# Optimization experiments

Hardware: AMD Instinct MI355X
Metric: run time of the kernel (lower is better)

## Reference

```python
import jax, jax.numpy as jnp
import numpy as np

B, L = 128, 128            # batch, num_features (sequence length)
D_MODEL = 256
D_INNER = 512              # expand=2
D_STATE = 16
D_CONV = 4
DT_RANK = 16               # ceil(d_model/16)
N_LAYERS = 2
LN_EPS = 1e-5


def setup_inputs() -> dict:
    key = jax.random.key(0)
    ks = jax.random.split(key, 12)
    rn = lambda k, shp, s=0.02: (jax.random.normal(k, shp, jnp.float32) * s)
    A_init = jnp.tile(jnp.arange(1, D_STATE + 1, dtype=jnp.float32), (N_LAYERS, D_INNER, 1))
    return {
        "x_num": jax.random.normal(ks[0], (B, L), jnp.float32),
        "scalar_w": rn(ks[1], (D_MODEL, 1), 0.5),
        "scalar_b": jnp.zeros((D_MODEL,), jnp.float32),
        "in_proj_w": rn(ks[2], (N_LAYERS, 2 * D_INNER, D_MODEL)),
        "conv_w": rn(ks[3], (N_LAYERS, D_INNER, D_CONV), 0.2),
        "conv_b": jnp.zeros((N_LAYERS, D_INNER), jnp.float32),
        "x_proj_w": rn(ks[4], (N_LAYERS, DT_RANK + 2 * D_STATE, D_INNER)),
        "dt_proj_w": rn(ks[5], (N_LAYERS, D_INNER, DT_RANK), 0.1),
        "dt_proj_b": jnp.full((N_LAYERS, D_INNER), float(np.log(np.expm1(0.01))), jnp.float32),
        "A_log": jnp.log(A_init),
        "D_skip": jnp.ones((N_LAYERS, D_INNER), jnp.float32),
        "out_proj_w": rn(ks[6], (N_LAYERS, D_MODEL, D_INNER)),
        "ln_g": jnp.ones((D_MODEL,), jnp.float32),
        "ln_b": jnp.zeros((D_MODEL,), jnp.float32),
        "h1_w": rn(ks[7], (D_MODEL, D_MODEL)),
        "h1_b": jnp.zeros((D_MODEL,), jnp.float32),
        "h2_w": rn(ks[8], (1, D_MODEL)),
        "h2_b": jnp.zeros((1,), jnp.float32),
    }


def _selective_scan(u, delta, A, Bm, C, D_skip):
    # u, delta: [B,L,Di]; A: [Di,N]; Bm, C: [B,L,N]
    deltaA = jnp.exp(jnp.einsum('bld,dn->bldn', delta, A))          # [B,L,Di,N]
    deltaBu = jnp.einsum('bld,bln,bld->bldn', delta, Bm, u)          # [B,L,Di,N]
    h0 = jnp.zeros((u.shape[0], u.shape[2], A.shape[1]), u.dtype)

    def step(h, inp):
        dA_t, dBu_t, c_t = inp
        h = dA_t * h + dBu_t                                         # [B,Di,N]
        y = jnp.einsum('bdn,bn->bd', h, c_t)
        return h, y

    _, ys = jax.lax.scan(
        step, h0,
        (deltaA.transpose(1, 0, 2, 3), deltaBu.transpose(1, 0, 2, 3), C.transpose(1, 0, 2)))
    return ys.transpose(1, 0, 2) + u * D_skip                        # [B,L,Di]


def _mamba_block(x, Wi, cw, cb, Wx, Wdt, bdt, A_log, Dsk, Wo):
    xz = jnp.einsum('bld,ed->ble', x, Wi)                            # [B,L,2*Di]
    xh, z = jnp.split(xz, 2, axis=-1)
    # causal depthwise conv1d, kernel D_CONV
    xt = xh.transpose(0, 2, 1)                                       # [B,Di,L]
    conv = jax.lax.conv_general_dilated(
        xt, cw[:, None, :], window_strides=(1,), padding=[(D_CONV - 1, 0)],
        feature_group_count=D_INNER)
    xh = jax.nn.silu((conv + cb[:, None]).transpose(0, 2, 1))        # [B,L,Di]
    x_dbl = jnp.einsum('bld,ed->ble', xh, Wx)                        # [B,L,DT_RANK+2N]
    dt, Bm, C = jnp.split(x_dbl, [DT_RANK, DT_RANK + D_STATE], axis=-1)
    delta = jax.nn.softplus(jnp.einsum('blr,dr->bld', dt, Wdt) + bdt)
    A = -jnp.exp(A_log)
    y = _selective_scan(xh, delta, A, Bm, C, Dsk)
    y = y * jax.nn.silu(z)
    return jnp.einsum('bld,od->blo', y, Wo)                          # [B,L,D_MODEL]


def reference(x_num, scalar_w, scalar_b, in_proj_w, conv_w, conv_b, x_proj_w,
              dt_proj_w, dt_proj_b, A_log, D_skip, out_proj_w, ln_g, ln_b,
              h1_w, h1_b, h2_w, h2_b):
    # scalar_proj: Linear(1, d_model) applied to each feature value
    x = x_num[:, :, None] * scalar_w[:, 0] + scalar_b                # [B,L,D_MODEL]
    for i in range(N_LAYERS):
        x = _mamba_block(x, in_proj_w[i], conv_w[i], conv_b[i], x_proj_w[i],
                         dt_proj_w[i], dt_proj_b[i], A_log[i], D_skip[i], out_proj_w[i])
    mu = x.mean(-1, keepdims=True)
    var = ((x - mu) ** 2).mean(-1, keepdims=True)
    x = (x - mu) * jax.lax.rsqrt(var + LN_EPS) * ln_g + ln_b
    pooled = x.mean(axis=1)                                          # [B,D_MODEL]
    h = jax.nn.gelu(pooled @ h1_w.T + h1_b, approximate=False)
    return (h @ h2_w.T + h2_b)[:, 0]                                 # [B]
```

## Files before the change

### kernel.cpp

```cpp
#include <hip/hip_runtime.h>
#include <math.h>

#define BB 128
#define LL 128
#define DM 256
#define DI 512
#define NS 16
#define MR (BB*LL)
#define SC 8
#define ST 16
#define EPAD 34

typedef unsigned short u16;
typedef __attribute__((ext_vector_type(8))) short bf16x8;
typedef __attribute__((ext_vector_type(8))) short us8;
typedef __attribute__((ext_vector_type(4))) short u16x4;
typedef __attribute__((ext_vector_type(4))) float f32x4;
typedef __attribute__((ext_vector_type(2))) float f32x2;

__device__ __forceinline__ u16 f2bf(float v) {
    unsigned u = __float_as_uint(v);
    return (u16)((u + 0x7fffu + ((u >> 16) & 1u)) >> 16);
}
__device__ __forceinline__ u16 ftoh(float v) {
    _Float16 h = (_Float16)v;
    return __builtin_bit_cast(unsigned short, h);
}
__device__ __forceinline__ float htof(u16 x) {
    return (float)__builtin_bit_cast(_Float16, x);
}

__device__ __forceinline__ void g2l16(const u16* g, u16* l) {
    __builtin_amdgcn_global_load_lds(
        (const __attribute__((address_space(1))) void*)g,
        (__attribute__((address_space(3))) void*)l,
        16, 0, 0);
}

__device__ __forceinline__ void unpack8(const f32x4& a, const f32x4& b,
                                        const f32x4& c, const f32x4& d, f32x2* o) {
    o[0]=(f32x2){a[0],a[1]}; o[1]=(f32x2){a[2],a[3]};
    o[2]=(f32x2){b[0],b[1]}; o[3]=(f32x2){b[2],b[3]};
    o[4]=(f32x2){c[0],c[1]}; o[5]=(f32x2){c[2],c[3]};
    o[6]=(f32x2){d[0],d[1]}; o[7]=(f32x2){d[2],d[3]};
}

__device__ __forceinline__ void pow_tree2(float r, f32x2* p2) {
    float q = r*r, s = q*q, t = s*s;
    p2[0] = (f32x2){r, q};
    f32x2 qq = (f32x2){q, q}, ss = (f32x2){s, s}, tt = (f32x2){t, t};
    p2[1] = p2[0]*qq;
    p2[2] = p2[0]*ss;
    p2[3] = p2[1]*ss;
    p2[4] = p2[0]*tt;
    p2[5] = p2[1]*tt;
    p2[6] = p2[2]*tt;
    p2[7] = p2[3]*tt;
}

__device__ __forceinline__ void store8h(const float* v, u16* dh) {
    bf16x8 hv;
    #pragma unroll
    for (int j = 0; j < 8; j++) hv[j] = (short)f2bf(v[j]);
    *(bf16x8*)dh = hv;
}

__device__ __forceinline__ void unswz(int id, int NB, int& nb, int& mb) {
    int low = id & 7, rest = id >> 3;
    nb = rest % NB;
    mb = ((rest / NB) << 3) | low;
}

__device__ __forceinline__ void ldfA(const u16* gA, int t, int quad, int wm, int r16,
                                     bf16x8* fa) {
    const u16* p = gA + (size_t)((t*4 + quad)*128)*8;
    #pragma unroll
    for (int mt = 0; mt < 4; mt++)
        fa[mt] = *(const bf16x8*)(p + (size_t)(wm*64 + mt*16 + r16)*8);
}
__device__ __forceinline__ void ldfB(const u16* gB, int t, int quad, int wn, int boff,
                                     int r16, bf16x8* fb) {
    const u16* p = gB + (size_t)((t*4 + quad)*128 + boff)*8;
    #pragma unroll
    for (int nt = 0; nt < 2; nt++)
        fb[nt] = *(const bf16x8*)(p + (size_t)(wn*32 + nt*16 + r16)*8);
}

#define NCI  32768
#define NCXT 8192
#define NCDT 2048
#define NCO  16384
#define NCZ  32768
#define NPREP_PACK (NCI + 2*NCXT + 2*NCDT + 2*NCO + NCZ)
#define PREP_BLOCKS (NPREP_PACK/256 + 512)
#define OFF_WI1  0
#define OFF_WXT0 262144
#define OFF_WXT1 327680
#define OFF_WDT0 393216
#define OFF_WDT1 409600
#define OFF_WO1  425984
#define OFF_WOT0 557056
__global__ __launch_bounds__(256) void k_prep(
    const float* __restrict__ sw, const float* __restrict__ sbias,
    const float* __restrict__ Wi_all, const float* __restrict__ Wx_all,
    const float* __restrict__ Wdt_all, const float* __restrict__ Wo_all,
    u16* __restrict__ wbase, u16* __restrict__ t16, float* __restrict__ wvbv)
{
    int gc = blockIdx.x * 256 + threadIdx.x;
    float v[8];
    u16* dh;
    if (gc < NCI) {
        int c = gc, m = c & 127, t = c >> 7, kc = t & 31, rb = t >> 5;
        const float* Wi = Wi_all + (size_t)1024*256;
        const float* p = Wi + (size_t)(rb*128 + m)*256 + kc*8;
        float4 a = *(const float4*)p, b = *(const float4*)(p+4);
        v[0]=a.x; v[1]=a.y; v[2]=a.z; v[3]=a.w; v[4]=b.x; v[5]=b.y; v[6]=b.z; v[7]=b.w;
        dh = wbase + OFF_WI1 + (size_t)c*8;
    } else if (gc < NCI + 2*NCXT) {
        int c = gc - NCI; int layer = (c >= NCXT); c -= layer*NCXT;
        int m = c & 127, kc = c >> 7;
        const float* Wx = Wx_all + (size_t)layer*48*512;
        #pragma unroll
        for (int j = 0; j < 8; j++) v[j] = (m < 48) ? Wx[(size_t)m*512 + kc*8 + j] : 0.f;
        dh = wbase + (layer ? OFF_WXT1 : OFF_WXT0) + (size_t)c*8;
    } else if (gc < NCI + 2*NCXT + 2*NCDT) {
        int c = gc - NCI - 2*NCXT; int layer = (c >= NCDT); c -= layer*NCDT;
        int m = c & 127, t = c >> 7, kc = t & 3, rb = t >> 2;
        int d = rb*128 + m;
        const float* Wdt = Wdt_all + (size_t)layer*512*16;
        #pragma unroll
        for (int j = 0; j < 8; j++) {
            int r = kc*8 + j;
            v[j] = (r < 16) ? Wdt[d*16 + r] : 0.f;
        }
        dh = wbase + (layer ? OFF_WDT1 : OFF_WDT0) + (size_t)c*8;
    } else if (gc < NCI + 2*NCXT + 2*NCDT + NCO) {
        int c = gc - NCI - 2*NCXT - 2*NCDT;
        int m = c & 127, t = c >> 7, kc = t & 63, rb = t >> 6;
        const float* Wo = Wo_all + (size_t)256*512;
        const float* p = Wo + (size_t)(rb*128 + m)*512 + kc*8;
        float4 a = *(const float4*)p, b = *(const float4*)(p+4);
        v[0]=a.x; v[1]=a.y; v[2]=a.z; v[3]=a.w; v[4]=b.x; v[5]=b.y; v[6]=b.z; v[7]=b.w;
        dh = wbase + OFF_WO1 + (size_t)c*8;
    } else if (gc < NCI + 2*NCXT + 2*NCDT + 2*NCO) {
        int c = gc - NCI - 2*NCXT - 2*NCDT - NCO;
        int m = c & 127, t = c >> 7, kc = t & 31, rb = t >> 5;
        int d = rb*128 + m;
        const float* Wo = Wo_all;
        #pragma unroll
        for (int j = 0; j < 8; j++) v[j] = Wo[(size_t)(kc*8 + j)*512 + d];
        dh = wbase + OFF_WOT0 + (size_t)c*8;
    } else if (gc < NPREP_PACK) {
        int c = gc - (NCI + 2*NCXT + 2*NCDT + 2*NCO);
        int mb = c >> 8, rem = c & 255;
        #pragma unroll
        for (int j = 0; j < 8; j++) v[j] = 0.f;
        dh = t16 + ((size_t)(mb*4 + 2)*128 + rem)*8;
    } else {
        int wb   = blockIdx.x - NPREP_PACK/256;
        int o    = wb*4 + (threadIdx.x >> 6);
        int lane = threadIdx.x & 63;
        int isB  = o >> 10, e = o & 1023;
        const float* vec = isB ? sbias : sw;
        const float* row = Wi_all + (size_t)e*256;
        float4 w4 = *(const float4*)&row[lane*4];
        float4 v4 = *(const float4*)&vec[lane*4];
        float a = w4.x*v4.x + w4.y*v4.y + w4.z*v4.z + w4.w*v4.w;
        #pragma unroll
        for (int off = 32; off > 0; off >>= 1) a += __shfl_down(a, off, 64);
        if (lane == 0) wvbv[isB*1024 + e] = a;
        return;
    }
    store8h(v, dh);
}

__global__ __launch_bounds__(256) void k_front0(
    const float* __restrict__ xn, const float* __restrict__ wvbv,
    const float* __restrict__ cw, const float* __restrict__ cb,
    u16* __restrict__ Yh, u16* __restrict__ u2, u16* __restrict__ z2)
{
    const int id = blockIdx.x;
    const int low = id & 7, rest = id >> 3;
    const int seg = rest >> 4;
    const int b   = ((rest & 15) << 3) | low;
    const int tid = threadIdx.x;
    const int l = tid & 127, sub = tid >> 7;
    const float* xb = xn + (size_t)b * LL;
    const float x0  = xb[l];
    const float xm1 = (l >= 1) ? xb[l-1] : 0.f;
    const float xm2 = (l >= 2) ? xb[l-2] : 0.f;
    const float xm3 = (l >= 3) ? xb[l-3] : 0.f;
    const float* wv = wvbv;
    const float* bv = wvbv + 1024;
    if (seg < 4) {
        const int kcb = (seg*128 + sub*64) >> 3;
        #pragma unroll 1
        for (int kk = 0; kk < 8; kk++) {
            const int kc = kcb + kk;
            float uv[8];
            #pragma unroll
            for (int q = 0; q < 8; q++) {
                int d = kc*8 + q;
                float4 c4 = *(const float4*)&cw[d*4];
                float conv = c4.x*xm3 + c4.y*xm2 + c4.z*xm1 + c4.w*x0;
                float cs = c4.w;
                if (l >= 1) cs += c4.z;
                if (l >= 2) cs += c4.y;
                if (l >= 3) cs += c4.x;
                float s = wv[d]*conv + bv[d]*cs + cb[d];
                float sig = 1.f/(1.f + __expf(-s));
                uv[q] = s*sig;
                u2[((size_t)b*512 + d)*128 + l] = ftoh(uv[q]);
            }
            store8h(uv, &Yh[(((size_t)b*64 + kc)*128 + l)*8]);
        }
    } else {
        const int d0 = (seg - 4)*128 + sub*64;
        #pragma unroll 1
        for (int dd = 0; dd < 64; dd++) {
            int d = d0 + dd;
            float s = x0*wv[512 + d] + bv[512 + d];
            z2[((size_t)b*512 + d)*128 + l] = ftoh(s);
        }
    }
}

template<int CM>
__global__ __launch_bounds__(256) void k_gemm_mfma(
    const u16* __restrict__ Ah, const u16* __restrict__ Bh,
    void* __restrict__ Cv, void* __restrict__ C2v,
    const float* __restrict__ bdt,
    int K, int Nvalid, int nsplit, int ldc, int ldc2, int NB)
{
    const int tid = threadIdx.x, lane = tid & 63, w = tid >> 6;
    const int wm = w >> 1, wn = w & 1;
    const int r16 = lane & 15, quad = lane >> 4;
    int nb, mb;
    unswz(blockIdx.x, NB, nb, mb);
    const int K8 = K >> 3;
    const int NT = K >> 5;

    f32x4 acc[4][2];
    #pragma unroll
    for (int mt = 0; mt < 4; mt++)
        #pragma unroll
        for (int nt = 0; nt < 2; nt++) acc[mt][nt] = (f32x4){0.f,0.f,0.f,0.f};

    const u16* gAh = Ah + (size_t)mb * K8 * 128 * 8;
    const int rbB = nb >> 1, boff = (nb & 1) * 64;
    const u16* gBh = Bh + (size_t)rbB * K8 * 128 * 8;

    bf16x8 fa0[4], fb0[2], fa1[4], fb1[2];
    ldfA(gAh, 0, quad, wm, r16, fa0);
    ldfB(gBh, 0, quad, wn, boff, r16, fb0);
    for (int t = 0; t < NT; t += 2) {
        if (t + 1 < NT) {
            ldfA(gAh, t+1, quad, wm, r16, fa1);
            ldfB(gBh, t+1, quad, wn, boff, r16, fb1);
        }
        #pragma unroll
        for (int mt = 0; mt < 4; mt++)
            #pragma unroll
            for (int nt = 0; nt < 2; nt++)
                acc[mt][nt] = __builtin_amdgcn_mfma_f32_16x16x32_bf16(fa0[mt], fb0[nt], acc[mt][nt], 0, 0, 0);
        if (t + 2 < NT) {
            ldfA(gAh, t+2, quad, wm, r16, fa0);
            ldfB(gBh, t+2, quad, wn, boff, r16, fb0);
        }
        if (t + 1 < NT) {
            #pragma unroll
            for (int mt = 0; mt < 4; mt++)
                #pragma unroll
                for (int nt = 0; nt < 2; nt++)
                    acc[mt][nt] = __builtin_amdgcn_mfma_f32_16x16x32_bf16(fa1[mt], fb1[nt], acc[mt][nt], 0, 0, 0);
        }
    }

    const int col0 = nb*64 + wn*32;
    #pragma unroll
    for (int mt = 0; mt < 4; mt++) {
        int lrow = wm*64 + mt*16 + quad*4;
        int rowb = mb*128 + lrow;
        #pragma unroll
        for (int nt = 0; nt < 2; nt++) {
            int col = col0 + nt*16 + r16;
            if (col < Nvalid) {
                if (CM != 2 && col >= nsplit) {
                    float* Cd = (float*)C2v; int cc = col - nsplit;
                    #pragma unroll
                    for (int r = 0; r < 4; r++)
                        Cd[(size_t)(rowb + r)*ldc2 + cc] = acc[mt][nt][r];
                } else if (CM == 1) {
                    u16* Cd = (u16*)Cv;
                    float bv = bdt[col];
                    u16x4 pd;
                    #pragma unroll
                    for (int r = 0; r < 4; r++) {
                        float v    = acc[mt][nt][r] + bv;
                        float expv = __expf(v);
                        float dlt  = (v > 20.f) ? v : __logf(1.f + expv);
                        pd[r] = (short)ftoh(dlt);
                    }
                    *(u16x4*)&Cd[((size_t)mb*512 + col)*128 + lrow] = pd;
                } else if (CM == 2) {
                    u16* Dh = (u16*)Cv;
                    size_t cb = ((size_t)mb*(size_t)ldc + (col>>3))*1024 + (col&7);
                    #pragma unroll
                    for (int r = 0; r < 4; r++)
                        Dh[cb + (size_t)(lrow + r)*8] = f2bf(acc[mt][nt][r]);
                } else if (CM == 3) {
                    u16* Dh = (u16*)Cv;
                    size_t cb = (size_t)mb*4096 + (size_t)(col>>3)*1024 + (col&7);
                    #pragma unroll
                    for (int r = 0; r < 4; r++)
                        Dh[cb + (size_t)(lrow + r)*8] = f2bf(acc[mt][nt][r]);
                } else {
                    float* Cd = (float*)Cv;
                    #pragma unroll
                    for (int r = 0; r < 4; r++)
                        Cd[(size_t)(rowb + r)*ldc + col] = acc[mt][nt][r];
                }
            }
        }
    }
}

__global__ __launch_bounds__(256) void k_gemm_in(
    const u16* __restrict__ Ah, const u16* __restrict__ Bh,
    const float* __restrict__ cw, const float* __restrict__ cb,
    u16* __restrict__ Yh, u16* __restrict__ u2, u16* __restrict__ z2, int K8c)
{
    __shared__ __align__(16) char smem[24576];
    u16* sAh = (u16*)smem;
    u16* sBh = (u16*)(smem + 16384);

    const int tid = threadIdx.x, lane = tid & 63, w = tid >> 6;
    const int wm = w >> 1, wn = w & 1;
    const int r16 = lane & 15, quad = lane >> 4;
    int nb, mb;
    unswz(blockIdx.x, 16, nb, mb);
    const int NT = K8c >> 2;

    f32x4 acc[4][2];
    #pragma unroll
    for (int mt = 0; mt < 4; mt++)
        #pragma unroll
        for (int nt = 0; nt < 2; nt++) acc[mt][nt] = (f32x4){0.f,0.f,0.f,0.f};

    const u16* gAh = Ah + (size_t)mb * K8c * 128 * 8;
    const int rbB = nb >> 1, boff = (nb & 1) * 64;
    const u16* gBh = Bh + (size_t)rbB * K8c * 128 * 8;

    {
        #pragma unroll
        for (int t = 0; t < 2; t++) {
            int s = w + t * 4;
            g2l16(gAh + (size_t)(s*64 + lane)*8, &sAh[(s*64 + lane)*8]);
        }
        g2l16(gBh + ((size_t)w*128 + boff + lane)*8, &sBh[(w*64 + lane)*8]);
    }

    int cur = 0;
    for (int t = 0; t < NT; t++) {
        __syncthreads();
        if (t + 1 < NT) {
            const int kc0 = (t + 1) * 4;
            const u16* ga = gAh + (size_t)kc0 * 128 * 8;
            u16* dA = sAh + (cur ^ 1) * 4096;
            u16* dB = sBh + (cur ^ 1) * 2048;
            #pragma unroll
            for (int tt = 0; tt < 2; tt++) {
                int s = w + tt * 4;
                g2l16(ga + (size_t)(s*64 + lane)*8, &dA[(s*64 + lane)*8]);
            }
            g2l16(gBh + ((size_t)(kc0 + w)*128 + boff + lane)*8, &dB[(w*64 + lane)*8]);
        }

        const u16* rA = sAh + cur * 4096;
        const u16* rB = sBh + cur * 2048;
        bf16x8 fa_h[4], fb_h[2];
        #pragma unroll
        for (int mt = 0; mt < 4; mt++) {
            int ch = quad*128 + wm*64 + mt*16 + r16;
            fa_h[mt] = *(const bf16x8*)&rA[ch*8];
        }
        #pragma unroll
        for (int nt = 0; nt < 2; nt++) {
            int ch = quad*64 + wn*32 + nt*16 + r16;
            fb_h[nt] = *(const bf16x8*)&rB[ch*8];
        }
        #pragma unroll
        for (int mt = 0; mt < 4; mt++)
            #pragma unroll
            for (int nt = 0; nt < 2; nt++)
                acc[mt][nt] = __builtin_amdgcn_mfma_f32_16x16x32_bf16(fa_h[mt], fb_h[nt], acc[mt][nt], 0, 0, 0);
        cur ^= 1;
    }

    if (nb < 8) {
        float* eps = (float*)smem;
        float* scw = (float*)(smem + 17408);
        float* scb = (float*)(smem + 18432);
        __syncthreads();
        if (tid < 256) scw[tid] = cw[nb*256 + tid];
        if (tid < 64)  scb[tid] = cb[nb*64 + tid];

        #pragma unroll
        for (int rr = 0; rr < 2; rr++) {
            if (wn == rr) {
                #pragma unroll
                for (int mt = 0; mt < 4; mt++) {
                    int rbase = wm*64 + mt*16 + quad*4;
                    #pragma unroll
                    for (int ntl = 0; ntl < 2; ntl++) {
                        int ct = ntl*16 + r16;
                        #pragma unroll
                        for (int r = 0; r < 4; r++)
                            eps[(rbase + r)*EPAD + ct] = acc[mt][ntl][r];
                    }
                }
            }
            __syncthreads();
            #pragma unroll
            for (int t = 0; t < 2; t++) {
                int l  = (tid & 31) + ((tid >> 5) & 3) * 32;
                int oo = (tid >> 7) + t*2;
                int dl_ = rr*32 + oo*8;
                float xr[4][8];
                #pragma unroll
                for (int r2 = 0; r2 < 4; r2++) {
                    int row = l - 3 + r2;
                    if (row >= 0) {
                        const float2* p = (const float2*)&eps[row*EPAD + oo*8];
                        float2 a = p[0], b2 = p[1], c2 = p[2], d2 = p[3];
                        xr[r2][0]=a.x; xr[r2][1]=a.y; xr[r2][2]=b2.x; xr[r2][3]=b2.y;
                        xr[r2][4]=c2.x; xr[r2][5]=c2.y; xr[r2][6]=d2.x; xr[r2][7]=d2.y;
                    } else {
                        #pragma unroll
                        for (int j = 0; j < 8; j++) xr[r2][j] = 0.f;
                    }
                }
                float uv[8];
                #pragma unroll
                for (int j = 0; j < 8; j++) {
                    int dj = dl_ + j;
                    float4 w4 = *(const float4*)&scw[dj*4];
                    float s = scb[dj] + w4.x*xr[0][j] + w4.y*xr[1][j]
                                      + w4.z*xr[2][j] + w4.w*xr[3][j];
                    float sig = 1.f/(1.f + __expf(-s));
                    uv[j] = s*sig;
                }
                int d = nb*64 + dl_;
                size_t base = ((size_t)(mb*64 + (d>>3))*128 + l)*8;
                store8h(uv, &Yh[base]);
                #pragma unroll
                for (int j = 0; j < 8; j++)
                    u2[((size_t)mb*512 + d + j)*128 + l] = ftoh(uv[j]);
            }
            __syncthreads();
        }
    } else {
        const int col0 = (nb-8)*64 + wn*32;
        #pragma unroll
        for (int mt = 0; mt < 4; mt++) {
            int lb = wm*64 + mt*16 + quad*4;
            #pragma unroll
            for (int nt = 0; nt < 2; nt++) {
                int d = col0 + nt*16 + r16;
                u16x4 pk;
                #pragma unroll
                for (int r = 0; r < 4; r++) pk[r] = (short)ftoh(acc[mt][nt][r]);
                *(u16x4*)&z2[((size_t)mb*512 + d)*128 + lb] = pk;
            }
        }
    }
}

__global__ __launch_bounds__(512, 8) void k_scan_fused(
    const u16* __restrict__ dls, const float* __restrict__ bc,
    const u16* __restrict__ uu, const u16* __restrict__ zz,
    const float* __restrict__ Dsk, u16* __restrict__ Yh)
{
    __shared__ float sR[SC][64];
    __shared__ float sH[SC][64*17];
    const int tid  = threadIdx.x;
    const int lane = tid & 63;
    const int c    = __builtin_amdgcn_readfirstlane(tid >> 6);
    const int id   = blockIdx.x;
    const int low  = id & 7, rest = id >> 3;
    const int dgrp = rest >> 4;
    const int b    = ((rest & 15) << 3) | low;
    const int d    = dgrp*64 + lane;
    const int l0   = c*ST;

    const float dsk = Dsk[d];
    const size_t tb = ((size_t)b*512 + d)*128 + l0;
    const u16* pd = dls + tb;
    const u16* up = uu + tb;
    const u16* zp = zz + tb;
    const size_t ybase = ((size_t)(b*64 + (d>>3))*128 + l0)*8 + (d&7);
    const float* bp = bc + ((size_t)b*LL + l0)*32;

    f32x2 h2[8];
    #pragma unroll
    for (int n = 0; n < 8; n++) h2[n] = (f32x2){0.f, 0.f};
    float R = 1.f;

    #pragma unroll 1
    for (int t8 = 0; t8 < ST/8; t8++) {
        us8 vd = *(const us8*)(pd + t8*8);
        us8 vu = *(const us8*)(up + t8*8);
        #pragma unroll
        for (int j = 0; j < 8; j++) {
            int t = t8*8 + j;
            const float* bpt = bp + t*32;
            f32x4 qa = *(const f32x4*)(bpt);
            f32x4 qb = *(const f32x4*)(bpt + 4);
            f32x4 qc = *(const f32x4*)(bpt + 8);
            f32x4 qd = *(const f32x4*)(bpt + 12);
            f32x2 bvv[8];
            unpack8(qa, qb, qc, qd, bvv);
            float dlt = htof((u16)vd[j]);
            float r1  = __expf(-dlt);
            float du  = dlt * htof((u16)vu[j]);
            R *= r1;
            f32x2 p2[8];
            pow_tree2(r1, p2);
            f32x2 du2 = (f32x2){du, du};
            #pragma unroll
            for (int n = 0; n < 8; n++) h2[n] = p2[n]*h2[n] + bvv[n]*du2;
        }
    }

    sR[c][lane] = R;
    #pragma unroll
    for (int n = 0; n < 8; n++) {
        sH[c][lane*17 + 2*n]     = h2[n][0];
        sH[c][lane*17 + 2*n + 1] = h2[n][1];
    }
    __syncthreads();
    f32x2 hin2[8];
    #pragma unroll
    for (int n = 0; n < 8; n++) hin2[n] = (f32x2){0.f, 0.f};
    for (int cc = 0; cc < c; cc++) {
        float Rv = sR[cc][lane];
        f32x2 P2[8];
        pow_tree2(Rv, P2);
        #pragma unroll
        for (int n = 0; n < 8; n++) {
            f32x2 Sv = (f32x2){sH[cc][lane*17 + 2*n], sH[cc][lane*17 + 2*n + 1]};
            hin2[n] = P2[n]*hin2[n] + Sv;
        }
    }

    #pragma unroll
    for (int n = 0; n < 8; n++) h2[n] = hin2[n];

    u16* ph = Yh + ybase;

    #pragma unroll 1
    for (int t8 = 0; t8 < ST/8; t8++) {
        us8 vd = *(const us8*)(pd + t8*8);
        us8 vu = *(const us8*)(up + t8*8);
        us8 vz = *(const us8*)(zp + t8*8);
        #pragma unroll
        for (int j = 0; j < 8; j++) {
            int t = t8*8 + j;
            const float* bpt = bp + t*32;
            f32x4 qa = *(const f32x4*)(bpt);
            f32x4 qb = *(const f32x4*)(bpt + 4);
            f32x4 qc = *(const f32x4*)(bpt + 8);
            f32x4 qd = *(const f32x4*)(bpt + 12);
            f32x4 qe = *(const f32x4*)(bpt + 16);
            f32x4 qf = *(const f32x4*)(bpt + 20);
            f32x4 qg = *(const f32x4*)(bpt + 24);
            f32x4 qh = *(const f32x4*)(bpt + 28);
            f32x2 bvv[8], cvv[8];
            unpack8(qa, qb, qc, qd, bvv);
            unpack8(qe, qf, qg, qh, cvv);
            float dlt = htof((u16)vd[j]);
            float r1  = __expf(-dlt);
            float u   = htof((u16)vu[j]);
            float zv  = htof((u16)vz[j]);
            float du  = dlt * u;
            f32x2 p2[8];
            pow_tree2(r1, p2);
            f32x2 du2 = (f32x2){du, du};
            f32x2 yv2 = (f32x2){0.f, 0.f};
            #pragma unroll
            for (int n = 0; n < 8; n++) {
                h2[n] = p2[n]*h2[n] + bvv[n]*du2;
                yv2  += h2[n]*cvv[n];
            }
            float yv = yv2[0] + yv2[1] + u * dsk;
            float sig = 1.f/(1.f + __expf(-zv));
            float yg = yv * (zv * sig);
            ph[(size_t)t*8] = f2bf(yg);
        }
    }
}

__global__ __launch_bounds__(256) void k_ln_head(const float* __restrict__ x,
    const float* __restrict__ g, const float* __restrict__ bt,
    const float* __restrict__ h1w, const float* __restrict__ h1b,
    const float* __restrict__ h2w, const float* __restrict__ h2b,
    float* __restrict__ out)
{
    __shared__ float4 part[4][64];
    __shared__ float sp[DM];
    __shared__ float sred[DM];
    int b = blockIdx.x, tid = threadIdx.x, wave = tid >> 6, lane = tid & 63;
    const float4* xp = (const float4*)(x + (size_t)b*LL*DM);
    float4 acc = make_float4(0.f, 0.f, 0.f, 0.f);
    for (int i = 0; i < 32; i++) {
        int l = wave*32 + i;
        float4 v = xp[l*64 + lane];
        float s  = v.x + v.y + v.z + v.w;
        float s2 = v.x*v.x + v.y*v.y + v.z*v.z + v.w*v.w;
        #pragma unroll
        for (int off = 32; off > 0; off >>= 1) {
            s  += __shfl_down(s,  off, 64);
            s2 += __shfl_down(s2, off, 64);
        }
        s  = __shfl(s,  0, 64);
        s2 = __shfl(s2, 0, 64);
        float mu  = s  * (1.f/DM);
        float var = s2 * (1.f/DM) - mu*mu;
        float rs  = rsqrtf(var + 1e-5f);
        acc.x += (v.x - mu)*rs;
        acc.y += (v.y - mu)*rs;
        acc.z += (v.z - mu)*rs;
        acc.w += (v.w - mu)*rs;
    }
    part[wave][lane] = acc;
    __syncthreads();
    if (wave == 0) {
        float4 a0 = part[0][lane], a1 = part[1][lane], a2 = part[2][lane], a3 = part[3][lane];
        float4 gv = ((const float4*)g)[lane];
        float4 bv = ((const float4*)bt)[lane];
        float4 o;
        o.x = (a0.x+a1.x+a2.x+a3.x)*(1.f/LL)*gv.x + bv.x;
        o.y = (a0.y+a1.y+a2.y+a3.y)*(1.f/LL)*gv.y + bv.y;
        o.z = (a0.z+a1.z+a2.z+a3.z)*(1.f/LL)*gv.z + bv.z;
        o.w = (a0.w+a1.w+a2.w+a3.w)*(1.f/LL)*gv.w + bv.w;
        *(float4*)&sp[lane*4] = o;
    }
    __syncthreads();
    int j = tid;
    float a = h1b[j];
    const float* wr = &h1w[(size_t)j*DM];
    for (int m = 0; m < DM; m += 4) {
        float4 w4 = *(const float4*)&wr[m];
        a += sp[m]*w4.x + sp[m+1]*w4.y + sp[m+2]*w4.z + sp[m+3]*w4.w;
    }
    float hg = 0.5f*a*(1.f + erff(a*0.70710678118654752440f));
    sred[j] = hg * h2w[j];
    __syncthreads();
    for (int s = 128; s > 0; s >>= 1) {
        if (j < s) sred[j] += sred[j+s];
        __syncthreads();
    }
    if (j == 0) out[b] = sred[0] + h2b[0];
}

extern "C" void kernel_launch(void* const* d_in, const int* in_sizes, int n_in,
                              void* d_out, int out_size, void* d_ws, size_t ws_size,
                              hipStream_t stream)
{
    const float* x_num    = (const float*)d_in[0];
    const float* scalar_w = (const float*)d_in[1];
    const float* scalar_b = (const float*)d_in[2];
    const float* in_proj  = (const float*)d_in[3];
    const float* conv_w   = (const float*)d_in[4];
    const float* conv_b   = (const float*)d_in[5];
    const float* x_proj   = (const float*)d_in[6];
    const float* dt_w     = (const float*)d_in[7];
    const float* dt_b     = (const float*)d_in[8];
    const float* D_skip   = (const float*)d_in[10];
    const float* out_proj = (const float*)d_in[11];
    const float* ln_g     = (const float*)d_in[12];
    const float* ln_b     = (const float*)d_in[13];
    const float* h1_w     = (const float*)d_in[14];
    const float* h1_b     = (const float*)d_in[15];
    const float* h2_w     = (const float*)d_in[16];
    const float* h2_b     = (const float*)d_in[17];
    float* out = (float*)d_out;

    float* ws      = (float*)d_ws;
    float* x_buf   = ws;
    float* xh_raw  = x_buf  + (size_t)MR*DM;
    float* z_buf   = xh_raw + (size_t)MR*DI;
    float* xh      = z_buf  + (size_t)MR*DI;
    float* xdbl    = xh     + (size_t)MR*DI;
    float* wsplit  = xdbl   + (size_t)MR*48;

    u16* u2   = (u16*)(xh + (size_t)MR*256);
    u16* AhX  = (u16*)xh_raw;
    u16* z2   = (u16*)z_buf;
    u16* Yh1  = (u16*)z_buf + (size_t)MR*512;
    u16* dl2  = (u16*)x_buf;
    float* bc = xdbl;
    u16* t16  = (u16*)(xdbl + (size_t)MR*32);

    u16* wbase   = (u16*)wsplit;
    float* extra = wsplit + 344064;
    u16* Wcomb   = (u16*)extra;
    float* wvbv  = extra + 262144;

    const int BIG = 1 << 30;

    k_prep<<<PREP_BLOCKS, 256, 0, stream>>>(
        scalar_w, scalar_b, in_proj, x_proj, dt_w, out_proj, wbase, t16, wvbv);

    k_gemm_mfma<2><<<64, 256, 0, stream>>>(
        wbase + OFF_WI1, wbase + OFF_WOT0, (void*)Wcomb, (void*)0, (const float*)0,
        256, 512, BIG, 64 , 0, 8);

    k_front0<<<BB*8, 256, 0, stream>>>(
        x_num, wvbv, conv_w, conv_b, AhX, u2, z2);

    k_gemm_mfma<3><<<128, 256, 0, stream>>>(
        AhX, wbase + OFF_WXT0, (void*)t16, (void*)bc, (const float*)0,
        512, 48, 16, 0, 32, 1);
    k_gemm_mfma<1><<<8*BB, 256, 0, stream>>>(
        t16, wbase + OFF_WDT0, (void*)dl2, (void*)0, dt_b,
        32, 512, BIG, 512, 32, 8);

    k_scan_fused<<<BB*8, 512, 0, stream>>>(dl2, bc, u2, z2, D_skip, AhX);

    k_gemm_in<<<16*BB, 256, 0, stream>>>(
        AhX, Wcomb, conv_w + (size_t)DI*4, conv_b + DI,
        Yh1, u2, z2, 64);

    k_gemm_mfma<3><<<128, 256, 0, stream>>>(
        Yh1, wbase + OFF_WXT1, (void*)t16, (void*)bc, (const float*)0,
        512, 48, 16, 0, 32, 1);
    k_gemm_mfma<1><<<8*BB, 256, 0, stream>>>(
        t16, wbase + OFF_WDT1, (void*)dl2, (void*)0, dt_b + DI,
        32, 512, BIG, 512, 32, 8);

    k_scan_fused<<<BB*8, 512, 0, stream>>>(dl2, bc, u2, z2, D_skip + DI, AhX);

    k_gemm_mfma<0><<<4*BB, 256, 0, stream>>>(
        AhX, wbase + OFF_WO1, (void*)x_buf, (void*)x_buf, (const float*)0,
        512, 256, BIG, 256, 256, 4);

    k_ln_head<<<BB, 256, 0, stream>>>(x_buf, ln_g, ln_b, h1_w, h1_b, h2_w, h2_b, out);
}
```

Baseline: 293.7 us.

## Fuse dt projection and softplus into selective scan kernel

Drops the separate MFMA GEMM that computed delta (dt_proj plus softplus) into a bf16 buffer. The x_proj GEMM now writes the dt-rank features as fp32, and each scan thread computes its 16 delta values with a rank-16 dot product against its dt_proj row. It also derives exp(-delta) as 1/(1+e^v), which saves one exp. This removes a kernel launch per layer and a delta round-trip through memory, at the cost of recomputing delta in both scan passes and more per-thread loads and registers.

```diff
diff --git a/kernel.cpp b/kernel.cpp
--- a/kernel.cpp
+++ b/kernel.cpp
@@ -88,23 +88,19 @@
 
 #define NCI  32768
 #define NCXT 8192
-#define NCDT 2048
 #define NCO  16384
-#define NCZ  32768
-#define NPREP_PACK (NCI + 2*NCXT + 2*NCDT + 2*NCO + NCZ)
+#define NPREP_PACK (NCI + 2*NCXT + 2*NCO)
 #define PREP_BLOCKS (NPREP_PACK/256 + 512)
 #define OFF_WI1  0
 #define OFF_WXT0 262144
 #define OFF_WXT1 327680
-#define OFF_WDT0 393216
-#define OFF_WDT1 409600
-#define OFF_WO1  425984
-#define OFF_WOT0 557056
+#define OFF_WO1  393216
+#define OFF_WOT0 524288
 __global__ __launch_bounds__(256) void k_prep(
     const float* __restrict__ sw, const float* __restrict__ sbias,
     const float* __restrict__ Wi_all, const float* __restrict__ Wx_all,
-    const float* __restrict__ Wdt_all, const float* __restrict__ Wo_all,
-    u16* __restrict__ wbase, u16* __restrict__ t16, float* __restrict__ wvbv)
+    const float* __restrict__ Wo_all,
+    u16* __restrict__ wbase, float* __restrict__ wvbv)
 {
     int gc = blockIdx.x * 256 + threadIdx.x;
     float v[8];
@@ -123,39 +119,22 @@
         #pragma unroll
         for (int j = 0; j < 8; j++) v[j] = (m < 48) ? Wx[(size_t)m*512 + kc*8 + j] : 0.f;
         dh = wbase + (layer ? OFF_WXT1 : OFF_WXT0) + (size_t)c*8;
-    } else if (gc < NCI + 2*NCXT + 2*NCDT) {
-        int c = gc - NCI - 2*NCXT; int layer = (c >= NCDT); c -= layer*NCDT;
-        int m = c & 127, t = c >> 7, kc = t & 3, rb = t >> 2;
-        int d = rb*128 + m;
-        const float* Wdt = Wdt_all + (size_t)layer*512*16;
-        #pragma unroll
-        for (int j = 0; j < 8; j++) {
-            int r = kc*8 + j;
-            v[j] = (r < 16) ? Wdt[d*16 + r] : 0.f;
-        }
-        dh = wbase + (layer ? OFF_WDT1 : OFF_WDT0) + (size_t)c*8;
-    } else if (gc < NCI + 2*NCXT + 2*NCDT + NCO) {
-        int c = gc - NCI - 2*NCXT - 2*NCDT;
+    } else if (gc < NCI + 2*NCXT + NCO) {
+        int c = gc - NCI - 2*NCXT;
         int m = c & 127, t = c >> 7, kc = t & 63, rb = t >> 6;
         const float* Wo = Wo_all + (size_t)256*512;
         const float* p = Wo + (size_t)(rb*128 + m)*512 + kc*8;
         float4 a = *(const float4*)p, b = *(const float4*)(p+4);
         v[0]=a.x; v[1]=a.y; v[2]=a.z; v[3]=a.w; v[4]=b.x; v[5]=b.y; v[6]=b.z; v[7]=b.w;
         dh = wbase + OFF_WO1 + (size_t)c*8;
-    } else if (gc < NCI + 2*NCXT + 2*NCDT + 2*NCO) {
-        int c = gc - NCI - 2*NCXT - 2*NCDT - NCO;
+    } else if (gc < NPREP_PACK) {
+        int c = gc - NCI - 2*NCXT - NCO;
         int m = c & 127, t = c >> 7, kc = t & 31, rb = t >> 5;
         int d = rb*128 + m;
         const float* Wo = Wo_all;
         #pragma unroll
         for (int j = 0; j < 8; j++) v[j] = Wo[(size_t)(kc*8 + j)*512 + d];
         dh = wbase + OFF_WOT0 + (size_t)c*8;
-    } else if (gc < NPREP_PACK) {
-        int c = gc - (NCI + 2*NCXT + 2*NCDT + 2*NCO);
-        int mb = c >> 8, rem = c & 255;
-        #pragma unroll
-        for (int j = 0; j < 8; j++) v[j] = 0.f;
-        dh = t16 + ((size_t)(mb*4 + 2)*128 + rem)*8;
     } else {
         int wb   = blockIdx.x - NPREP_PACK/256;
         int o    = wb*4 + (threadIdx.x >> 6);
@@ -229,7 +208,6 @@
 __global__ __launch_bounds__(256) void k_gemm_mfma(
     const u16* __restrict__ Ah, const u16* __restrict__ Bh,
     void* __restrict__ Cv, void* __restrict__ C2v,
-    const float* __restrict__ bdt,
     int K, int Nvalid, int nsplit, int ldc, int ldc2, int NB)
 {
     const int tid = threadIdx.x, lane = tid & 63, w = tid >> 6;
@@ -290,27 +268,9 @@
                     #pragma unroll
                     for (int r = 0; r < 4; r++)
                         Cd[(size_t)(rowb + r)*ldc2 + cc] = acc[mt][nt][r];
-                } else if (CM == 1) {
-                    u16* Cd = (u16*)Cv;
-                    float bv = bdt[col];
-                    u16x4 pd;
-                    #pragma unroll
-                    for (int r = 0; r < 4; r++) {
-                        float v    = acc[mt][nt][r] + bv;
-                        float expv = __expf(v);
-                        float dlt  = (v > 20.f) ? v : __logf(1.f + expv);
-                        pd[r] = (short)ftoh(dlt);
-                    }
-                    *(u16x4*)&Cd[((size_t)mb*512 + col)*128 + lrow] = pd;
                 } else if (CM == 2) {
                     u16* Dh = (u16*)Cv;
                     size_t cb = ((size_t)mb*(size_t)ldc + (col>>3))*1024 + (col&7);
-                    #pragma unroll
-                    for (int r = 0; r < 4; r++)
-                        Dh[cb + (size_t)(lrow + r)*8] = f2bf(acc[mt][nt][r]);
-                } else if (CM == 3) {
-                    u16* Dh = (u16*)Cv;
-                    size_t cb = (size_t)mb*4096 + (size_t)(col>>3)*1024 + (col&7);
                     #pragma unroll
                     for (int r = 0; r < 4; r++)
                         Dh[cb + (size_t)(lrow + r)*8] = f2bf(acc[mt][nt][r]);
@@ -477,7 +437,8 @@
 }
 
 __global__ __launch_bounds__(512, 8) void k_scan_fused(
-    const u16* __restrict__ dls, const float* __restrict__ bc,
+    const float* __restrict__ t16f, const float* __restrict__ wdt,
+    const float* __restrict__ bdt, const float* __restrict__ bc,
     const u16* __restrict__ uu, const u16* __restrict__ zz,
     const float* __restrict__ Dsk, u16* __restrict__ Yh)
 {
@@ -495,24 +456,52 @@
 
     const float dsk = Dsk[d];
     const size_t tb = ((size_t)b*512 + d)*128 + l0;
-    const u16* pd = dls + tb;
     const u16* up = uu + tb;
     const u16* zp = zz + tb;
     const size_t ybase = ((size_t)(b*64 + (d>>3))*128 + l0)*8 + (d&7);
     const float* bp = bc + ((size_t)b*LL + l0)*32;
 
+    float v16[16];
+    {
+        const float* wrow = wdt + (size_t)d*16;
+        f32x4 w0 = *(const f32x4*)(wrow);
+        f32x4 w1 = *(const f32x4*)(wrow + 4);
+        f32x4 w2 = *(const f32x4*)(wrow + 8);
+        f32x4 w3 = *(const f32x4*)(wrow + 12);
+        const float bd = bdt[d];
+        const float* tp = t16f + ((size_t)b*LL + l0)*16;
+        #pragma unroll
+        for (int t = 0; t < ST; t++) {
+            f32x4 q0 = *(const f32x4*)(tp + t*16);
+            f32x4 q1 = *(const f32x4*)(tp + t*16 + 4);
+            f32x4 q2 = *(const f32x4*)(tp + t*16 + 8);
+            f32x4 q3 = *(const f32x4*)(tp + t*16 + 12);
+            float v = bd;
+            v += q0[0]*w0[0] + q0[1]*w0[1] + q0[2]*w0[2] + q0[3]*w0[3];
+            v += q1[0]*w1[0] + q1[1]*w1[1] + q1[2]*w1[2] + q1[3]*w1[3];
+            v += q2[0]*w2[0] + q2[1]*w2[1] + q2[2]*w2[2] + q2[3]*w2[3];
+            v += q3[0]*w3[0] + q3[1]*w3[1] + q3[2]*w3[2] + q3[3]*w3[3];
+            v16[t] = v;
+        }
+    }
+
     f32x2 h2[8];
     #pragma unroll
     for (int n = 0; n < 8; n++) h2[n] = (f32x2){0.f, 0.f};
     float R = 1.f;
 
-    #pragma unroll 1
-    for (int t8 = 0; t8 < ST/8; t8++) {
-        us8 vd = *(const us8*)(pd + t8*8);
-        us8 vu = *(const us8*)(up + t8*8);
-        #pragma unroll
-        for (int j = 0; j < 8; j++) {
-            int t = t8*8 + j;
+    {
+        us8 vu0 = *(const us8*)(up);
+        us8 vu1 = *(const us8*)(up + 8);
+        #pragma unroll
+        for (int t = 0; t < ST; t++) {
+            float u   = htof((u16)(t < 8 ? vu0[t] : vu1[t-8]));
+            float v   = v16[t];
+            float e   = __expf(v);
+            float dlt = (v > 80.f) ? v : __logf(1.f + e);
+            float r1  = 1.f / (1.f + e);
+            float du  = dlt * u;
+            R *= r1;
             const float* bpt = bp + t*32;
             f32x4 qa = *(const f32x4*)(bpt);
             f32x4 qb = *(const f32x4*)(bpt + 4);
@@ -520,10 +509,6 @@
             f32x4 qd = *(const f32x4*)(bpt + 12);
             f32x2 bvv[8];
             unpack8(qa, qb, qc, qd, bvv);
-            float dlt = htof((u16)vd[j]);
-            float r1  = __expf(-dlt);
-            float du  = dlt * htof((u16)vu[j]);
-            R *= r1;
             f32x2 p2[8];
             pow_tree2(r1, p2);
             f32x2 du2 = (f32x2){du, du};
@@ -557,15 +542,20 @@
     for (int n = 0; n < 8; n++) h2[n] = hin2[n];
 
     u16* ph = Yh + ybase;
-
-    #pragma unroll 1
-    for (int t8 = 0; t8 < ST/8; t8++) {
-        us8 vd = *(const us8*)(pd + t8*8);
-        us8 vu = *(const us8*)(up + t8*8);
-        us8 vz = *(const us8*)(zp + t8*8);
-        #pragma unroll
-        for (int j = 0; j < 8; j++) {
-            int t = t8*8 + j;
+    {
+        us8 vu0 = *(const us8*)(up);
+        us8 vu1 = *(const us8*)(up + 8);
+        us8 vz0 = *(const us8*)(zp);
+        us8 vz1 = *(const us8*)(zp + 8);
+        #pragma unroll
+        for (int t = 0; t < ST; t++) {
+            float u   = htof((u16)(t < 8 ? vu0[t] : vu1[t-8]));
+            float zv  = htof((u16)(t < 8 ? vz0[t] : vz1[t-8]));
+            float v   = v16[t];
+            float e   = __expf(v);
+            float dlt = (v > 80.f) ? v : __logf(1.f + e);
+            float r1  = 1.f / (1.f + e);
+            float du  = dlt * u;
             const float* bpt = bp + t*32;
             f32x4 qa = *(const f32x4*)(bpt);
             f32x4 qb = *(const f32x4*)(bpt + 4);
@@ -578,11 +568,6 @@
             f32x2 bvv[8], cvv[8];
             unpack8(qa, qb, qc, qd, bvv);
             unpack8(qe, qf, qg, qh, cvv);
-            float dlt = htof((u16)vd[j]);
-            float r1  = __expf(-dlt);
-            float u   = htof((u16)vu[j]);
-            float zv  = htof((u16)vz[j]);
-            float du  = dlt * u;
             f32x2 p2[8];
             pow_tree2(r1, p2);
             f32x2 du2 = (f32x2){du, du};
@@ -694,55 +679,50 @@
     float* xdbl    = xh     + (size_t)MR*DI;
     float* wsplit  = xdbl   + (size_t)MR*48;
 
-    u16* u2   = (u16*)(xh + (size_t)MR*256);
-    u16* AhX  = (u16*)xh_raw;
-    u16* z2   = (u16*)z_buf;
-    u16* Yh1  = (u16*)z_buf + (size_t)MR*512;
-    u16* dl2  = (u16*)x_buf;
-    float* bc = xdbl;
-    u16* t16  = (u16*)(xdbl + (size_t)MR*32);
+    u16* u2    = (u16*)(xh + (size_t)MR*256);
+    u16* AhX   = (u16*)xh_raw;
+    u16* z2    = (u16*)z_buf;
+    u16* Yh1   = (u16*)z_buf + (size_t)MR*512;
+    float* bc  = xdbl;
+    float* t16f = xdbl + (size_t)MR*32;
 
     u16* wbase   = (u16*)wsplit;
-    float* extra = wsplit + 344064;
+    float* extra = wsplit + 327680;
     u16* Wcomb   = (u16*)extra;
     float* wvbv  = extra + 262144;
 
     const int BIG = 1 << 30;
 
     k_prep<<<PREP_BLOCKS, 256, 0, stream>>>(
-        scalar_w, scalar_b, in_proj, x_proj, dt_w, out_proj, wbase, t16, wvbv);
+        scalar_w, scalar_b, in_proj, x_proj, out_proj, wbase, wvbv);
 
     k_gemm_mfma<2><<<64, 256, 0, stream>>>(
-        wbase + OFF_WI1, wbase + OFF_WOT0, (void*)Wcomb, (void*)0, (const float*)0,
+        wbase + OFF_WI1, wbase + OFF_WOT0, (void*)Wcomb, (void*)0,
         256, 512, BIG, 64 , 0, 8);
 
     k_front0<<<BB*8, 256, 0, stream>>>(
         x_num, wvbv, conv_w, conv_b, AhX, u2, z2);
 
-    k_gemm_mfma<3><<<128, 256, 0, stream>>>(
-        AhX, wbase + OFF_WXT0, (void*)t16, (void*)bc, (const float*)0,
-        512, 48, 16, 0, 32, 1);
-    k_gemm_mfma<1><<<8*BB, 256, 0, stream>>>(
-        t16, wbase + OFF_WDT0, (void*)dl2, (void*)0, dt_b,
-        32, 512, BIG, 512, 32, 8);
-
-    k_scan_fused<<<BB*8, 512, 0, stream>>>(dl2, bc, u2, z2, D_skip, AhX);
+    k_gemm_mfma<0><<<128, 256, 0, stream>>>(
+        AhX, wbase + OFF_WXT0, (void*)t16f, (void*)bc,
+        512, 48, 16, 16, 32, 1);
+
+    k_scan_fused<<<BB*8, 512, 0, stream>>>(
+        t16f, dt_w, dt_b, bc, u2, z2, D_skip, AhX);
 
     k_gemm_in<<<16*BB, 256, 0, stream>>>(
         AhX, Wcomb, conv_w + (size_t)DI*4, conv_b + DI,
         Yh1, u2, z2, 64);
 
-    k_gemm_mfma<3><<<128, 256, 0, stream>>>(
-        Yh1, wbase + OFF_WXT1, (void*)t16, (void*)bc, (const float*)0,
-        512, 48, 16, 0, 32, 1);
-    k_gemm_mfma<1><<<8*BB, 256, 0, stream>>>(
-        t16, wbase + OFF_WDT1, (void*)dl2, (void*)0, dt_b + DI,
-        32, 512, BIG, 512, 32, 8);
-
-    k_scan_fused<<<BB*8, 512, 0, stream>>>(dl2, bc, u2, z2, D_skip + DI, AhX);
+    k_gemm_mfma<0><<<128, 256, 0, stream>>>(
+        Yh1, wbase + OFF_WXT1, (void*)t16f, (void*)bc,
+        512, 48, 16, 16, 32, 1);
+
+    k_scan_fused<<<BB*8, 512, 0, stream>>>(
+        t16f, dt_w + (size_t)DI*16, dt_b + DI, bc, u2, z2, D_skip + DI, AhX);
 
     k_gemm_mfma<0><<<4*BB, 256, 0, stream>>>(
-        AhX, wbase + OFF_WO1, (void*)x_buf, (void*)x_buf, (const float*)0,
+        AhX, wbase + OFF_WO1, (void*)x_buf, (void*)x_buf,
         512, 256, BIG, 256, 256, 4);
 
     k_ln_head<<<BB, 256, 0, stream>>>(x_buf, ln_g, ln_b, h1_w, h1_b, h2_w, h2_b, out);
```

New measurement: 966.1 us. +228.9%, slower.
